# Optimization experiments

Hardware: AMD Instinct MI355X
Metric: run time of the kernel (lower is better)

## Reference

```python
import jax, jax.numpy as jnp
import numpy as np

NL, BS, NQ, D, NH, HD, L, P, DFF, NC = 6, 16, 300, 256, 8, 32, 3, 4, 1024, 80
SHAPES = np.array([[80, 80], [40, 40], [20, 20]], np.int32)  # (H, W) per level: 640x640 input, strides 8/16/32
STARTS = np.array([0, 6400, 8000], np.int32)
LV = 8400  # sum H*W


def setup_inputs():
    keys = iter(jax.random.split(jax.random.key(0), 64))

    def rn(shape, s=0.02):
        return jax.random.normal(next(keys), shape, jnp.float32) * s

    return {
        "tgt": rn((BS, NQ, D), 1.0),
        "ref_points_unact": rn((BS, NQ, 4), 1.0),
        "memory": rn((BS, LV, D), 1.0),
        "spatial_shapes": jnp.asarray(SHAPES),
        "level_start_index": jnp.asarray(STARTS),
        "Wq": rn((NL, D, D)), "bq": rn((NL, D)),
        "Wk": rn((NL, D, D)), "bk": rn((NL, D)),
        "Wv": rn((NL, D, D)), "bv": rn((NL, D)),
        "Wo": rn((NL, D, D)), "bo": rn((NL, D)),
        "ln1_g": jnp.ones((NL, D)), "ln1_b": jnp.zeros((NL, D)),
        "ln2_g": jnp.ones((NL, D)), "ln2_b": jnp.zeros((NL, D)),
        "ln3_g": jnp.ones((NL, D)), "ln3_b": jnp.zeros((NL, D)),
        "Wvp": rn((NL, D, D)), "bvp": rn((NL, D)),
        "Woff": rn((NL, D, NH * L * P * 2)), "boff": rn((NL, NH * L * P * 2), 0.5),
        "Waw": rn((NL, D, NH * L * P)), "baw": rn((NL, NH * L * P)),
        "Wop": rn((NL, D, D)), "bop": rn((NL, D)),
        "Wff1": rn((NL, D, DFF)), "bff1": rn((NL, DFF)),
        "Wff2": rn((NL, DFF, D)), "bff2": rn((NL, D)),
        "Wb1": rn((NL, D, D)), "bb1": rn((NL, D)),
        "Wb2": rn((NL, D, D)), "bb2": rn((NL, D)),
        "Wb3": rn((NL, D, 4)), "bb3": rn((NL, 4)),
        "Ws": rn((NL, D, NC)), "bs_": rn((NL, NC)),
        "Wp1": rn((4, 2 * D)), "bp1": rn((2 * D,)),
        "Wp2": rn((2 * D, D)), "bp2": rn((D,)),
    }


def _ln(x, g, b):
    m = x.mean(-1, keepdims=True)
    v = ((x - m) ** 2).mean(-1, keepdims=True)
    return (x - m) * jax.lax.rsqrt(v + 1e-5) * g + b


def _inv_sigmoid(x, eps=1e-5):
    x = jnp.clip(x, 0.0, 1.0)
    return jnp.log(jnp.clip(x, eps, None)) - jnp.log(jnp.clip(1.0 - x, eps, None))


def _forward(shapes, starts, tgt, ref_points_unact, memory, Wq, bq, Wk, bk, Wv, bv, Wo, bo, ln1_g, ln1_b, ln2_g, ln2_b, ln3_g, ln3_b, Wvp, bvp, Woff, boff, Waw, baw, Wop, bop, Wff1, bff1, Wff2, bff2, Wb1, bb1, Wb2, bb2, Wb3, bb3, Ws, bs_, Wp1, bp1, Wp2, bp2):
    bs, Lq, _ = tgt.shape

    def mha(q, k, v, i):
        qh = (q @ Wq[i] + bq[i]).reshape(bs, Lq, NH, HD)
        kh = (k @ Wk[i] + bk[i]).reshape(bs, Lq, NH, HD)
        vh = (v @ Wv[i] + bv[i]).reshape(bs, Lq, NH, HD)
        att = jax.nn.softmax(jnp.einsum('bqhd,bkhd->bhqk', qh, kh) / np.float32(np.sqrt(HD)), -1)
        return jnp.einsum('bhqk,bkhd->bqhd', att, vh).reshape(bs, Lq, D) @ Wo[i] + bo[i]

    def deform(query, ref, i):
        # multi-scale deformable attention (Deformable-DETR core, bilinear, zero padding)
        val = (memory @ Wvp[i] + bvp[i]).reshape(bs, -1, NH, HD).transpose(0, 2, 1, 3)  # [bs,NH,Lv,HD]
        off = (query @ Woff[i] + boff[i]).reshape(bs, Lq, NH, L, P, 2)
        aw = jax.nn.softmax((query @ Waw[i] + baw[i]).reshape(bs, Lq, NH, L * P), -1).reshape(bs, Lq, NH, L, P)
        r = ref[:, :, None, None, None, :]  # [bs,Lq,1,1,1,4] box (cx,cy,w,h)
        loc = r[..., :2] + off / P * r[..., 2:] * 0.5  # [bs,Lq,NH,L,P,2]
        out = jnp.zeros((bs, NH, Lq, HD), query.dtype)
        for lvl in range(L):
            H, W = int(shapes[lvl, 0]), int(shapes[lvl, 1])
            s = int(starts[lvl])
            vl = val[:, :, s:s + H * W]  # [bs,NH,H*W,HD]
            x = loc[:, :, :, lvl, :, 0].transpose(0, 2, 1, 3) * W - 0.5  # [bs,NH,Lq,P] (align_corners=False)
            y = loc[:, :, :, lvl, :, 1].transpose(0, 2, 1, 3) * H - 0.5
            x0 = jnp.floor(x).astype(jnp.int32)
            y0 = jnp.floor(y).astype(jnp.int32)
            wx, wy = x - x0, y - y0

            def g(xi, yi):
                valid = ((xi >= 0) & (xi < W) & (yi >= 0) & (yi < H)).astype(query.dtype)
                idx = jnp.clip(yi, 0, H - 1) * W + jnp.clip(xi, 0, W - 1)
                gat = jnp.take_along_axis(vl, idx.reshape(bs, NH, Lq * P, 1), axis=2)
                return gat.reshape(bs, NH, Lq, P, HD) * valid[..., None]

            samp = (g(x0, y0) * ((1 - wx) * (1 - wy))[..., None]
                    + g(x0 + 1, y0) * (wx * (1 - wy))[..., None]
                    + g(x0, y0 + 1) * ((1 - wx) * wy)[..., None]
                    + g(x0 + 1, y0 + 1) * (wx * wy)[..., None])
            awl = aw[:, :, :, lvl].transpose(0, 2, 1, 3)  # [bs,NH,Lq,P]
            out = out + (samp * awl[..., None]).sum(3)
        return out.transpose(0, 2, 1, 3).reshape(bs, Lq, D) @ Wop[i] + bop[i]

    ref_d = jax.nn.sigmoid(ref_points_unact)
    out = tgt
    bboxes = logits = None
    for i in range(NL):
        qpos = jax.nn.relu(ref_d @ Wp1 + bp1) @ Wp2 + bp2  # query_pos_head MLP(4 -> 512 -> 256)
        q = out + qpos
        out = _ln(out + mha(q, q, out, i), ln1_g[i], ln1_b[i])
        out = _ln(out + deform(out + qpos, ref_d, i), ln2_g[i], ln2_b[i])
        out = _ln(out + jax.nn.relu(out @ Wff1[i] + bff1[i]) @ Wff2[i] + bff2[i], ln3_g[i], ln3_b[i])
        h = jax.nn.relu(out @ Wb1[i] + bb1[i])
        h = jax.nn.relu(h @ Wb2[i] + bb2[i])
        inter = jax.nn.sigmoid(h @ Wb3[i] + bb3[i] + _inv_sigmoid(ref_d))
        if i == NL - 1:  # eval_idx = -1 -> outputs taken at last layer (inference path)
            bboxes = inter[None]
            logits = (out @ Ws[i] + bs_[i])[None]
        ref_d = inter
    return bboxes, logits


def reference(tgt, ref_points_unact, memory, spatial_shapes, level_start_index, Wq, bq, Wk, bk, Wv, bv, Wo, bo, ln1_g, ln1_b, ln2_g, ln2_b, ln3_g, ln3_b, Wvp, bvp, Woff, boff, Waw, baw, Wop, bop, Wff1, bff1, Wff2, bff2, Wb1, bb1, Wb2, bb2, Wb3, bb3, Ws, bs_, Wp1, bp1, Wp2, bp2):
    shapes = np.asarray(spatial_shapes)
    starts = np.asarray(level_start_index)
    return _forward(shapes, starts, tgt, ref_points_unact, memory, Wq, bq, Wk, bk, Wv, bv, Wo, bo, ln1_g, ln1_b, ln2_g, ln2_b, ln3_g, ln3_b, Wvp, bvp, Woff, boff, Waw, baw, Wop, bop, Wff1, bff1, Wff2, bff2, Wb1, bb1, Wb2, bb2, Wb3, bb3, Ws, bs_, Wp1, bp1, Wp2, bp2)
```

## Files before the change

kernel.cpp:

```cpp
#include <hip/hip_runtime.h>

#define NLAYERS 6
#define BSZ 16
#define NQL 300
#define DM 256
#define NHEAD 8
#define HDIM 32
#define NLVL 3
#define NPT 4
#define DFFN 1024
#define NCLS 80
#define LVTOT 8400
#define NROW (BSZ * NQL)
#define MEMN (BSZ * LVTOT)

typedef __attribute__((ext_vector_type(8))) short bf16x8;
typedef __attribute__((ext_vector_type(8))) ushort us8;
typedef __attribute__((ext_vector_type(4))) float f32x4;

__device__ __forceinline__ float b2f(ushort u) {
    return __uint_as_float(((uint)u) << 16);
}
__device__ __forceinline__ ushort f2b(float f) {
    uint i = __float_as_uint(f);
    uint r = i + 0x7fffu + ((i >> 16) & 1u);
    return (ushort)(r >> 16);
}
__device__ __forceinline__ void split2(float v, ushort& h, ushort& l) {
    ushort hh = f2b(v);
    h = hh;
    l = f2b(v - b2f(hh));
}
__device__ __forceinline__ void gl_lds16(const void* g, void* l) {
    __builtin_amdgcn_global_load_lds(
        (const __attribute__((address_space(1))) unsigned int*)g,
        (__attribute__((address_space(3))) unsigned int*)l, 16, 0, 0);
}

__global__ __launch_bounds__(256) void f2b_kernel(
    const float* __restrict__ src, ushort* __restrict__ dst, int n)
{
    int i = (blockIdx.x * 256 + threadIdx.x) * 4;
    if (i < n) {
        float4 v = *(const float4*)&src[i];
        ushort4 o = {f2b(v.x), f2b(v.y), f2b(v.z), f2b(v.w)};
        *(ushort4*)&dst[i] = o;
    }
}

__global__ __launch_bounds__(256) void split_kernel(
    const float* __restrict__ src, ushort* __restrict__ dh,
    ushort* __restrict__ dl, int n)
{
    int i = (blockIdx.x * 256 + threadIdx.x) * 4;
    if (i < n) {
        float4 v = *(const float4*)&src[i];
        ushort4 h, l;
        split2(v.x, h.x, l.x);
        split2(v.y, h.y, l.y);
        split2(v.z, h.z, l.z);
        split2(v.w, h.w, l.w);
        *(ushort4*)&dh[i] = h;
        *(ushort4*)&dl[i] = l;
    }
}

#define NTE 14
struct TTab {
    const float* s[NTE];
    ushort* d[NTE];
    int K[NTE], N[NTE], dls[NTE], dr0[NTE];
    int tstart[NTE + 1];
};

__global__ __launch_bounds__(256) void transpose_batch_kernel(TTab tab)
{
    __shared__ float tile[32][33];
    const int bx = blockIdx.x;
    int e = 0;
    while (e < NTE - 1 && bx >= tab.tstart[e + 1]) ++e;
    const int local = bx - tab.tstart[e];
    const int K = tab.K[e], N = tab.N[e];
    const int tx_n = (N + 31) >> 5, ty_n = (K + 31) >> 5;
    const int perB = tx_n * ty_n;
    const int z = local / perB;
    const int rem = local - z * perB;
    const int tyi = rem / tx_n, txi = rem - tyi * tx_n;
    const float* src = tab.s[e] + (size_t)z * K * N;
    ushort* dh = tab.d[e] + (size_t)z * tab.dls[e] + (size_t)tab.dr0[e] * K;
    const int n0 = txi * 32, k0 = tyi * 32;
    const int tx = threadIdx.x, ty = threadIdx.y;
    for (int r = 0; r < 32; r += 8) {
        int k = k0 + ty + r, n = n0 + tx;
        if (k < K && n < N) tile[ty + r][tx] = src[(size_t)k * N + n];
    }
    __syncthreads();
    for (int r = 0; r < 32; r += 8) {
        int n = n0 + ty + r, k = k0 + tx;
        if (n < N && k < K) dh[(size_t)n * K + k] = f2b(tile[tx][ty + r]);
    }
}

__global__ __launch_bounds__(256) void concat_both_kernel(
    const float* __restrict__ bq, const float* __restrict__ bk, float* __restrict__ bqk,
    const float* __restrict__ boff, const float* __restrict__ baw, float* __restrict__ bfa)
{
    const int bx = blockIdx.x;
    if (bx < 12) {
        int i = bx * 256 + threadIdx.x;
        if (i < 6 * 512) {
            int l = i / 512, j = i - l * 512;
            bqk[i] = (j < 256) ? bq[l * 256 + j] : bk[l * 256 + j - 256];
        }
    } else {
        int i = (bx - 12) * 256 + threadIdx.x;
        if (i < 6 * 288) {
            int l = i / 288, j = i - l * 288;
            bfa[i] = (j < 192) ? boff[l * 192 + j] : baw[l * 96 + j - 192];
        }
    }
}

template <int ACT>
__global__ __launch_bounds__(256) void gemm_ps(
    const ushort* __restrict__ Ahp, const ushort* __restrict__ Alp,
    const ushort* __restrict__ BTh, const float* __restrict__ bias,
    int M, int N, int K,
    float* __restrict__ Cf, const float* __restrict__ addsrc,
    ushort* __restrict__ Ch, ushort* __restrict__ Cl)
{
    __shared__ __align__(16) ushort Ahs[2][64 * 32];
    __shared__ __align__(16) ushort Als[2][64 * 32];
    __shared__ __align__(16) ushort Bhs[2][64 * 32];

    const int tid  = threadIdx.x;
    const int m0   = blockIdx.x * 64;
    const int n0   = blockIdx.y * 64;
    const int wv   = tid >> 6;
    const int lane = tid & 63;
    const int lm   = lane & 15;
    const int lq   = lane >> 4;
    const int r    = tid >> 2;
    const int c8   = (tid & 3) * 8;

    gl_lds16(&Ahp[(size_t)(m0 + r) * K + c8], &Ahs[0][r * 32 + c8]);
    gl_lds16(&Alp[(size_t)(m0 + r) * K + c8], &Als[0][r * 32 + c8]);
    gl_lds16(&BTh[(size_t)(n0 + r) * K + c8], &Bhs[0][r * 32 + c8]);
    __syncthreads();

    f32x4 acc[4] = {};
    int buf = 0;
    for (int k0 = 32; k0 < K + 32; k0 += 32) {
        const int nxt = buf ^ 1;
        if (k0 < K) {
            gl_lds16(&Ahp[(size_t)(m0 + r) * K + k0 + c8], &Ahs[nxt][r * 32 + c8]);
            gl_lds16(&Alp[(size_t)(m0 + r) * K + k0 + c8], &Als[nxt][r * 32 + c8]);
            gl_lds16(&BTh[(size_t)(n0 + r) * K + k0 + c8], &Bhs[nxt][r * 32 + c8]);
        }
        bf16x8 afh = *(const bf16x8*)&Ahs[buf][(wv * 16 + lm) * 32 + lq * 8];
        bf16x8 afl = *(const bf16x8*)&Als[buf][(wv * 16 + lm) * 32 + lq * 8];
#pragma unroll
        for (int nb = 0; nb < 4; ++nb) {
            bf16x8 bfh = *(const bf16x8*)&Bhs[buf][(nb * 16 + lm) * 32 + lq * 8];
            acc[nb] = __builtin_amdgcn_mfma_f32_16x16x32_bf16(afh, bfh, acc[nb], 0, 0, 0);
            acc[nb] = __builtin_amdgcn_mfma_f32_16x16x32_bf16(afl, bfh, acc[nb], 0, 0, 0);
        }
        __syncthreads();
        buf = nxt;
    }

    const int row = m0 + wv * 16 + lq * 4;
#pragma unroll
    for (int nb = 0; nb < 4; ++nb) {
        int col = n0 + nb * 16 + lm;
        if (col < N) {
            float bv = bias ? bias[col] : 0.f;
#pragma unroll
            for (int rr = 0; rr < 4; ++rr) {
                float v = acc[nb][rr] + bv;
                if (ACT) v = fmaxf(v, 0.f);
                const size_t idx = (size_t)(row + rr) * N + col;
                if (Cf) Cf[idx] = v;
                if (Ch) {
                    float w = addsrc ? (v + addsrc[idx]) : v;
                    ushort h, l;
                    split2(w, h, l);
                    Ch[idx] = h;
                    if (Cl) Cl[idx] = l;
                }
            }
        }
    }
}

__global__ __launch_bounds__(256) void gemm_mix(
    const ushort* __restrict__ Ahp, const ushort* __restrict__ Alp,
    const ushort* __restrict__ BTh, const float* __restrict__ bias,
    int N, int K,
    float* __restrict__ Cf, const float* __restrict__ addsrc,
    ushort* __restrict__ Ch, ushort* __restrict__ Cl,
    int nSmall,
    const ushort* __restrict__ gA, const ushort* __restrict__ gB,
    const float* __restrict__ gbias, ushort* __restrict__ gC,
    int chunkOff)
{
    __shared__ __align__(16) ushort lds[12288];

    const int tid  = threadIdx.x;
    const int wv   = tid >> 6;
    const int lane = tid & 63;
    const int lm   = lane & 15;
    const int lq   = lane >> 4;

    if ((int)blockIdx.x < nSmall) {
        typedef ushort (*lds2)[64 * 32];
        lds2 Ahs = (lds2)lds;
        lds2 Als = (lds2)(lds + 4096);
        lds2 Bhs = (lds2)(lds + 8192);
        const int m0 = (blockIdx.x % 75) * 64;
        const int n0 = (blockIdx.x / 75) * 64;
        const int r  = tid >> 2;
        const int c8 = (tid & 3) * 8;

        gl_lds16(&Ahp[(size_t)(m0 + r) * K + c8], &Ahs[0][r * 32 + c8]);
        gl_lds16(&Alp[(size_t)(m0 + r) * K + c8], &Als[0][r * 32 + c8]);
        gl_lds16(&BTh[(size_t)(n0 + r) * K + c8], &Bhs[0][r * 32 + c8]);
        __syncthreads();

        f32x4 acc[4] = {};
        int buf = 0;
        for (int k0 = 32; k0 < K + 32; k0 += 32) {
            const int nxt = buf ^ 1;
            if (k0 < K) {
                gl_lds16(&Ahp[(size_t)(m0 + r) * K + k0 + c8], &Ahs[nxt][r * 32 + c8]);
                gl_lds16(&Alp[(size_t)(m0 + r) * K + k0 + c8], &Als[nxt][r * 32 + c8]);
                gl_lds16(&BTh[(size_t)(n0 + r) * K + k0 + c8], &Bhs[nxt][r * 32 + c8]);
            }
            bf16x8 afh = *(const bf16x8*)&Ahs[buf][(wv * 16 + lm) * 32 + lq * 8];
            bf16x8 afl = *(const bf16x8*)&Als[buf][(wv * 16 + lm) * 32 + lq * 8];
#pragma unroll
            for (int nb = 0; nb < 4; ++nb) {
                bf16x8 bfh = *(const bf16x8*)&Bhs[buf][(nb * 16 + lm) * 32 + lq * 8];
                acc[nb] = __builtin_amdgcn_mfma_f32_16x16x32_bf16(afh, bfh, acc[nb], 0, 0, 0);
                acc[nb] = __builtin_amdgcn_mfma_f32_16x16x32_bf16(afl, bfh, acc[nb], 0, 0, 0);
            }
            __syncthreads();
            buf = nxt;
        }

        const int row = m0 + wv * 16 + lq * 4;
#pragma unroll
        for (int nb = 0; nb < 4; ++nb) {
            int col = n0 + nb * 16 + lm;
            if (col < N) {
                float bv = bias[col];
#pragma unroll
                for (int rr = 0; rr < 4; ++rr) {
                    float v = acc[nb][rr] + bv;
                    const size_t idx = (size_t)(row + rr) * N + col;
                    if (Cf) Cf[idx] = v;
                    if (Ch) {
                        float w = addsrc ? (v + addsrc[idx]) : v;
                        ushort h, l;
                        split2(w, h, l);
                        Ch[idx] = h;
                        if (Cl) Cl[idx] = l;
                    }
                }
            }
        }
    } else {
        ushort* As = lds;
        ushort* Bs = lds + 4096;
        const int bid = (int)blockIdx.x - nSmall + chunkOff;
        const int n0 = (bid & 1) * 128;
        const int m0 = (bid >> 1) * 128;
        const int wr = wv >> 1, wc = wv & 1;
        const int srow = lane >> 2;
        const int scol = (lane & 3) * 8;

        f32x4 acc[4][4] = {};

        for (int k0 = 0; k0 < 256; k0 += 32) {
            __syncthreads();
#pragma unroll
            for (int s2 = 0; s2 < 2; ++s2) {
                const int seg = wv * 2 + s2;
                const int row = seg * 16 + srow;
                gl_lds16(&gA[(size_t)(m0 + row) * 256 + k0 + scol],
                         &As[seg * 512 + lane * 8]);
                gl_lds16(&gB[(size_t)(n0 + row) * 256 + k0 + scol],
                         &Bs[seg * 512 + lane * 8]);
            }
            __syncthreads();

            bf16x8 af[4], bfr[4];
#pragma unroll
            for (int i = 0; i < 4; ++i)
                af[i] = *(const bf16x8*)&As[(wr * 64 + i * 16 + lm) * 32 + lq * 8];
#pragma unroll
            for (int i = 0; i < 4; ++i)
                bfr[i] = *(const bf16x8*)&Bs[(wc * 64 + i * 16 + lm) * 32 + lq * 8];
#pragma unroll
            for (int mi = 0; mi < 4; ++mi)
#pragma unroll
                for (int ni = 0; ni < 4; ++ni)
                    acc[mi][ni] = __builtin_amdgcn_mfma_f32_16x16x32_bf16(
                        af[mi], bfr[ni], acc[mi][ni], 0, 0, 0);
        }

#pragma unroll
        for (int ni = 0; ni < 4; ++ni) {
            const int col = n0 + wc * 64 + ni * 16 + lm;
            const float bv = gbias[col];
#pragma unroll
            for (int mi = 0; mi < 4; ++mi) {
                const int row = m0 + wr * 64 + mi * 16 + lq * 4;
#pragma unroll
                for (int rr = 0; rr < 4; ++rr)
                    gC[(size_t)(row + rr) * 256 + col] = f2b(acc[mi][ni][rr] + bv);
            }
        }
    }
}

__global__ __launch_bounds__(256) void gemm_qkv(
    const ushort* __restrict__ qhp, const ushort* __restrict__ qlp,
    const ushort* __restrict__ ohp, const ushort* __restrict__ olp,
    const ushort* __restrict__ Bqk, const ushort* __restrict__ Bv,
    const float* __restrict__ biasqk, const float* __restrict__ biasv,
    ushort* __restrict__ Cqk, ushort* __restrict__ Cv)
{
    constexpr int K = 256;
    __shared__ __align__(16) ushort Ahs[2][64 * 32];
    __shared__ __align__(16) ushort Als[2][64 * 32];
    __shared__ __align__(16) ushort Bhs[2][64 * 32];

    const int by = blockIdx.y;
    const ushort *Ahp, *Alp, *BTh;
    const float* bias;
    ushort* Ch;
    int N, n0;
    if (by < 8) { Ahp = qhp; Alp = qlp; BTh = Bqk; bias = biasqk; Ch = Cqk; N = 512; n0 = by * 64; }
    else        { Ahp = ohp; Alp = olp; BTh = Bv;  bias = biasv;  Ch = Cv;  N = 256; n0 = (by - 8) * 64; }

    const int tid  = threadIdx.x;
    const int m0   = blockIdx.x * 64;
    const int wv   = tid >> 6;
    const int lane = tid & 63;
    const int lm   = lane & 15;
    const int lq   = lane >> 4;
    const int r    = tid >> 2;
    const int c8   = (tid & 3) * 8;

    gl_lds16(&Ahp[(size_t)(m0 + r) * K + c8], &Ahs[0][r * 32 + c8]);
    gl_lds16(&Alp[(size_t)(m0 + r) * K + c8], &Als[0][r * 32 + c8]);
    gl_lds16(&BTh[(size_t)(n0 + r) * K + c8], &Bhs[0][r * 32 + c8]);
    __syncthreads();

    f32x4 acc[4] = {};
    int buf = 0;
    for (int k0 = 32; k0 < K + 32; k0 += 32) {
        const int nxt = buf ^ 1;
        if (k0 < K) {
            gl_lds16(&Ahp[(size_t)(m0 + r) * K + k0 + c8], &Ahs[nxt][r * 32 + c8]);
            gl_lds16(&Alp[(size_t)(m0 + r) * K + k0 + c8], &Als[nxt][r * 32 + c8]);
            gl_lds16(&BTh[(size_t)(n0 + r) * K + k0 + c8], &Bhs[nxt][r * 32 + c8]);
        }
        bf16x8 afh = *(const bf16x8*)&Ahs[buf][(wv * 16 + lm) * 32 + lq * 8];
        bf16x8 afl = *(const bf16x8*)&Als[buf][(wv * 16 + lm) * 32 + lq * 8];
#pragma unroll
        for (int nb = 0; nb < 4; ++nb) {
            bf16x8 bfh = *(const bf16x8*)&Bhs[buf][(nb * 16 + lm) * 32 + lq * 8];
            acc[nb] = __builtin_amdgcn_mfma_f32_16x16x32_bf16(afh, bfh, acc[nb], 0, 0, 0);
            acc[nb] = __builtin_amdgcn_mfma_f32_16x16x32_bf16(afl, bfh, acc[nb], 0, 0, 0);
        }
        __syncthreads();
        buf = nxt;
    }

    const int row = m0 + wv * 16 + lq * 4;
#pragma unroll
    for (int nb = 0; nb < 4; ++nb) {
        const int col = n0 + nb * 16 + lm;
        const float bv = bias[col];
#pragma unroll
        for (int rr = 0; rr < 4; ++rr)
            Ch[(size_t)(row + rr) * N + col] = f2b(acc[nb][rr] + bv);
    }
}

__global__ __launch_bounds__(256) void mha_mfma_kernel(
    const ushort* __restrict__ qh, int ldq, const ushort* __restrict__ kh, int ldk,
    const ushort* __restrict__ vh, int ldv,
    ushort* __restrict__ outh, ushort* __restrict__ outl)
{
    __shared__ ushort Kh[304 * 36];
    __shared__ ushort Vth[32 * 328];
    __shared__ ushort Pb[4][16 * 168];

    const int tid = threadIdx.x;
    const int wv = tid >> 6, lane = tid & 63;
    const int bh = blockIdx.x >> 1, half = blockIdx.x & 1;
    const int b = bh >> 3, h = bh & 7;
    const size_t qbase = (size_t)b * NQL * ldq + h * HDIM;
    const size_t kbase = (size_t)b * NQL * ldk + h * HDIM;
    const size_t vbase = (size_t)b * NQL * ldv + h * HDIM;
    const size_t obase = (size_t)b * NQL * DM + h * HDIM;

    for (int idx = tid; idx < 304 * 32; idx += 256) {
        int row = idx >> 5, d = idx & 31;
        Kh[row * 36 + d] = (row < NQL) ? kh[kbase + (size_t)row * ldk + d] : (ushort)0;
    }
    for (int idx = tid; idx < 328 * 32; idx += 256) {
        int key = idx >> 5, d = idx & 31;
        Vth[d * 328 + key] = (key < NQL) ? vh[vbase + (size_t)key * ldv + d] : (ushort)0;
    }
    for (int i = lane; i < 16 * 168; i += 64) Pb[wv][i] = 0;
    __syncthreads();

    const int quad = lane >> 4, c = lane & 15;
    const float scale = 0.17677669529663687f;

    const int qt_beg = (half ? 10 : 0) + wv;
    const int qt_end = (half ? 19 : 10);
    for (int qt = qt_beg; qt < qt_end; qt += 4) {
        const int q = qt * 16 + c;
        bf16x8 qf = *(const bf16x8*)&qh[qbase + (size_t)q * ldq + quad * 8];

        f32x4 sc[19];
#pragma unroll
        for (int kt = 0; kt < 19; ++kt) {
            bf16x8 kf = *(const bf16x8*)&Kh[(kt * 16 + c) * 36 + quad * 8];
            f32x4 a = {};
            a = __builtin_amdgcn_mfma_f32_16x16x32_bf16(qf, kf, a, 0, 0, 0);
            sc[kt] = a;
        }
        float inv4[4];
#pragma unroll
        for (int r = 0; r < 4; ++r) {
            float mx = -1e30f;
#pragma unroll
            for (int kt = 0; kt < 19; ++kt) {
                float s = sc[kt][r] * scale;
                if (kt * 16 + c >= NQL) s = -1e30f;
                sc[kt][r] = s;
                mx = fmaxf(mx, s);
            }
#pragma unroll
            for (int m = 1; m < 16; m <<= 1) mx = fmaxf(mx, __shfl_xor(mx, m, 64));
            float l = 0.f;
#pragma unroll
            for (int kt = 0; kt < 19; ++kt) {
                float p = __expf(sc[kt][r] - mx);
                sc[kt][r] = p;
                l += p;
            }
#pragma unroll
            for (int m = 1; m < 16; m <<= 1) l += __shfl_xor(l, m, 64);
            inv4[r] = 1.f / l;
        }

        f32x4 o0 = {}, o1 = {};
#pragma unroll
        for (int r = 0; r < 4; ++r)
#pragma unroll
            for (int kt = 0; kt < 10; ++kt)
                Pb[wv][(quad * 4 + r) * 168 + kt * 16 + c] = f2b(sc[kt][r] * inv4[r]);
#pragma unroll
        for (int ks = 0; ks < 5; ++ks) {
            bf16x8 pf = *(const bf16x8*)&Pb[wv][c * 168 + ks * 32 + quad * 8];
            bf16x8 v0 = *(const bf16x8*)&Vth[c * 328 + ks * 32 + quad * 8];
            bf16x8 v1 = *(const bf16x8*)&Vth[(16 + c) * 328 + ks * 32 + quad * 8];
            o0 = __builtin_amdgcn_mfma_f32_16x16x32_bf16(pf, v0, o0, 0, 0, 0);
            o1 = __builtin_amdgcn_mfma_f32_16x16x32_bf16(pf, v1, o1, 0, 0, 0);
        }
#pragma unroll
        for (int r = 0; r < 4; ++r) {
#pragma unroll
            for (int kt = 10; kt < 19; ++kt)
                Pb[wv][(quad * 4 + r) * 168 + (kt - 10) * 16 + c] = f2b(sc[kt][r] * inv4[r]);
            Pb[wv][(quad * 4 + r) * 168 + 144 + c] = 0;
        }
#pragma unroll
        for (int ks = 0; ks < 5; ++ks) {
            bf16x8 pf = *(const bf16x8*)&Pb[wv][c * 168 + ks * 32 + quad * 8];
            bf16x8 v0 = *(const bf16x8*)&Vth[c * 328 + 160 + ks * 32 + quad * 8];
            bf16x8 v1 = *(const bf16x8*)&Vth[(16 + c) * 328 + 160 + ks * 32 + quad * 8];
            o0 = __builtin_amdgcn_mfma_f32_16x16x32_bf16(pf, v0, o0, 0, 0, 0);
            o1 = __builtin_amdgcn_mfma_f32_16x16x32_bf16(pf, v1, o1, 0, 0, 0);
        }
#pragma unroll
        for (int r = 0; r < 4; ++r) {
            const int qq = qt * 16 + quad * 4 + r;
            if (qq < NQL) {
                ushort hh, ll;
                split2(o0[r], hh, ll);
                outh[obase + (size_t)qq * DM + c] = hh;
                outl[obase + (size_t)qq * DM + c] = ll;
                split2(o1[r], hh, ll);
                outh[obase + (size_t)qq * DM + 16 + c] = hh;
                outl[obase + (size_t)qq * DM + 16 + c] = ll;
            }
        }
    }
}

__global__ __launch_bounds__(256) void deform_kernel(
    const ushort* __restrict__ val, const float* __restrict__ offaw,
    const float* __restrict__ refd,
    ushort* __restrict__ samph, ushort* __restrict__ sampl)
{
    __shared__ float offs[192];
    __shared__ float aws[96];
    __shared__ float rr[4];
    const int row = blockIdx.x;
    const int b = row / NQL;
    const int t = threadIdx.x;
    if (t < 192) offs[t] = offaw[(size_t)row * 288 + t];
    if (t < 96)  aws[t] = offaw[(size_t)row * 288 + 192 + t];
    if (t < 4)   rr[t] = refd[row * 4 + t];
    __syncthreads();

    const int h = t >> 5, d = t & 31;
    float mx = -1e30f;
#pragma unroll
    for (int j = 0; j < 12; ++j) mx = fmaxf(mx, aws[h * 12 + j]);
    float ev[12]; float se = 0.f;
#pragma unroll
    for (int j = 0; j < 12; ++j) { ev[j] = __expf(aws[h * 12 + j] - mx); se += ev[j]; }
    const float inv = 1.f / se;

    const int HWs[3] = {80, 40, 20};
    const int STs[3] = {0, 6400, 8000};
    float acc = 0.f;
#pragma unroll
    for (int l = 0; l < NLVL; ++l) {
        const int Wd = HWs[l], Hd = HWs[l], st = STs[l];
#pragma unroll
        for (int p = 0; p < NPT; ++p) {
            const float w12 = ev[l * 4 + p] * inv;
            const float ox = offs[((h * 3 + l) * 4 + p) * 2 + 0];
            const float oy = offs[((h * 3 + l) * 4 + p) * 2 + 1];
            const float x = (rr[0] + ox * 0.125f * rr[2]) * Wd - 0.5f;
            const float y = (rr[1] + oy * 0.125f * rr[3]) * Hd - 0.5f;
            const float xf = floorf(x), yf = floorf(y);
            const int x0 = (int)xf, y0 = (int)yf;
            const float wx = x - xf, wy = y - yf;
            const float tw[4] = {(1 - wx) * (1 - wy), wx * (1 - wy),
                                 (1 - wx) * wy,       wx * wy};
            const int xs[4] = {x0, x0 + 1, x0, x0 + 1};
            const int ys[4] = {y0, y0, y0 + 1, y0 + 1};
            float sv = 0.f;
#pragma unroll
            for (int tp = 0; tp < 4; ++tp) {
                const int xi = xs[tp], yi = ys[tp];
                if (xi >= 0 && xi < Wd && yi >= 0 && yi < Hd) {
                    const int idx = st + yi * Wd + xi;
                    sv += tw[tp] * b2f(val[((size_t)b * LVTOT + idx) * DM + h * HDIM + d]);
                }
            }
            acc += w12 * sv;
        }
    }
    ushort hh, ll;
    split2(acc, hh, ll);
    samph[(size_t)row * DM + t] = hh;
    sampl[(size_t)row * DM + t] = ll;
}

__global__ __launch_bounds__(256) void addln_kernel(
    const float* x, const float* __restrict__ dl,
    const float* __restrict__ g, const float* __restrict__ bb,
    float* outf, ushort* __restrict__ outh, ushort* __restrict__ outl,
    const float* __restrict__ qpos, ushort* __restrict__ q2h, ushort* __restrict__ q2l)
{
    const int wv = threadIdx.x >> 6, lane = threadIdx.x & 63;
    const int row = blockIdx.x * 4 + wv;
    const size_t base = (size_t)row * DM + lane * 4;
    const float4 xv = *(const float4*)(x + base);
    const float4 dv = *(const float4*)(dl + base);
    float v[4] = {xv.x + dv.x, xv.y + dv.y, xv.z + dv.z, xv.w + dv.w};

    float s = v[0] + v[1] + v[2] + v[3];
#pragma unroll
    for (int m = 32; m; m >>= 1) s += __shfl_xor(s, m, 64);
    const float mean = s * (1.f / 256.f);
    float sq = 0.f;
#pragma unroll
    for (int j = 0; j < 4; ++j) { float dd = v[j] - mean; sq += dd * dd; }
#pragma unroll
    for (int m = 32; m; m >>= 1) sq += __shfl_xor(sq, m, 64);
    const float rstd = rsqrtf(sq * (1.f / 256.f) + 1e-5f);

    float y[4];
    ushort4 yh, yl;
#pragma unroll
    for (int j = 0; j < 4; ++j) {
        const int col = lane * 4 + j;
        y[j] = (v[j] - mean) * rstd * g[col] + bb[col];
    }
    *(float4*)(outf + base) = make_float4(y[0], y[1], y[2], y[3]);
    split2(y[0], yh.x, yl.x);
    split2(y[1], yh.y, yl.y);
    split2(y[2], yh.z, yl.z);
    split2(y[3], yh.w, yl.w);
    *(ushort4*)(outh + base) = yh;
    *(ushort4*)(outl + base) = yl;
    if (q2h) {
        const float4 qp = *(const float4*)(qpos + base);
        float q2v[4] = {y[0] + qp.x, y[1] + qp.y, y[2] + qp.z, y[3] + qp.w};
        ushort4 qh_, ql_;
        split2(q2v[0], qh_.x, ql_.x);
        split2(q2v[1], qh_.y, ql_.y);
        split2(q2v[2], qh_.z, ql_.z);
        split2(q2v[3], qh_.w, ql_.w);
        *(ushort4*)(q2h + base) = qh_;
        *(ushort4*)(q2l + base) = ql_;
    }
}

__global__ __launch_bounds__(256) void bbox_fused(
    const ushort* __restrict__ h2h, const ushort* __restrict__ h2l,
    const float* __restrict__ Wb3, const float* __restrict__ bb3,
    const float* __restrict__ rpu, float* __restrict__ refd,
    float* __restrict__ dout, int mode, int writeout,
    const float* __restrict__ Wp1, const float* __restrict__ bp1,
    ushort* __restrict__ t1h, ushort* __restrict__ t1l, int computeT1)
{
    __shared__ float hls[64 * 258];
    __shared__ float wb3s[1024];
    __shared__ float wp1s[4 * 512];
    __shared__ float bp1s[512];
    __shared__ float ref4[64 * 4];

    const int tid = threadIdx.x;
    const int r0 = blockIdx.x * 64;

    if (computeT1) {
        for (int i = tid; i < 2048; i += 256) wp1s[i] = Wp1[i];
        if (tid < 256) { bp1s[tid] = bp1[tid]; bp1s[tid + 256] = bp1[tid + 256]; }
    }
    if (mode == 1) {
        for (int i = tid; i < 1024; i += 256) wb3s[i] = Wb3[i];
        for (int j = tid; j < 2048; j += 256) {
            const int row = j >> 5, seg = (j & 31) * 8;
            const size_t g = (size_t)(r0 + row) * 256 + seg;
            us8 hv = *(const us8*)&h2h[g];
            us8 lv = *(const us8*)&h2l[g];
            float* o = &hls[row * 258 + seg];
#pragma unroll
            for (int x = 0; x < 8; ++x) o[x] = b2f(hv[x]) + b2f(lv[x]);
        }
    }
    __syncthreads();

    const int r = tid >> 2, c = tid & 3;
    float v;
    if (mode == 1) {
        float acc = 0.f;
        const float* hrow = &hls[r * 258];
#pragma unroll 4
        for (int k = 0; k < 256; ++k)
            acc = fmaf(hrow[k], wb3s[k * 4 + c], acc);
        const float b3v = acc + bb3[c];
        const float old = refd[(size_t)(r0 + r) * 4 + c];
        const float rc = fminf(fmaxf(old, 0.f), 1.f);
        const float invs = logf(fmaxf(rc, 1e-5f)) - logf(fmaxf(1.f - rc, 1e-5f));
        v = 1.f / (1.f + __expf(-(b3v + invs)));
    } else {
        v = 1.f / (1.f + __expf(-rpu[(size_t)(r0 + r) * 4 + c]));
    }
    refd[(size_t)(r0 + r) * 4 + c] = v;
    if (writeout) dout[(size_t)(r0 + r) * 4 + c] = v;
    ref4[r * 4 + c] = v;
    __syncthreads();

    if (!computeT1) return;
#pragma unroll
    for (int jj = 0; jj < 16; ++jj) {
        const int idx = jj * 2048 + tid * 8;
        const int row = idx >> 9, nb = idx & 511;
        const float a0 = ref4[row * 4 + 0], a1 = ref4[row * 4 + 1];
        const float a2 = ref4[row * 4 + 2], a3 = ref4[row * 4 + 3];
        us8 hv, lv;
#pragma unroll
        for (int x = 0; x < 8; ++x) {
            const int n = nb + x;
            float t = bp1s[n];
            t = fmaf(a0, wp1s[n], t);
            t = fmaf(a1, wp1s[512 + n], t);
            t = fmaf(a2, wp1s[1024 + n], t);
            t = fmaf(a3, wp1s[1536 + n], t);
            t = fmaxf(t, 0.f);
            ushort hh, ll;
            split2(t, hh, ll);
            hv[x] = hh; lv[x] = ll;
        }
        const size_t gg = (size_t)(r0 + row) * 512 + nb;
        *(us8*)&t1h[gg] = hv;
        *(us8*)&t1l[gg] = lv;
    }
}

extern "C" void kernel_launch(void* const* d_in, const int* in_sizes, int n_in,
                              void* d_out, int out_size, void* d_ws, size_t ws_size,
                              hipStream_t stream)
{
    const float* tgt    = (const float*)d_in[0];
    const float* rpu    = (const float*)d_in[1];
    const float* memory = (const float*)d_in[2];
    const float* Wq  = (const float*)d_in[5];  const float* bq  = (const float*)d_in[6];
    const float* Wk  = (const float*)d_in[7];  const float* bk  = (const float*)d_in[8];
    const float* Wv  = (const float*)d_in[9];  const float* bv  = (const float*)d_in[10];
    const float* Wo  = (const float*)d_in[11]; const float* bo  = (const float*)d_in[12];
    const float* ln1g = (const float*)d_in[13]; const float* ln1b = (const float*)d_in[14];
    const float* ln2g = (const float*)d_in[15]; const float* ln2b = (const float*)d_in[16];
    const float* ln3g = (const float*)d_in[17]; const float* ln3b = (const float*)d_in[18];
    const float* Wvp = (const float*)d_in[19]; const float* bvp = (const float*)d_in[20];
    const float* Woff = (const float*)d_in[21]; const float* boff = (const float*)d_in[22];
    const float* Waw = (const float*)d_in[23]; const float* baw = (const float*)d_in[24];
    const float* Wop = (const float*)d_in[25]; const float* bop = (const float*)d_in[26];
    const float* Wff1 = (const float*)d_in[27]; const float* bff1 = (const float*)d_in[28];
    const float* Wff2 = (const float*)d_in[29]; const float* bff2 = (const float*)d_in[30];
    const float* Wb1 = (const float*)d_in[31]; const float* bb1 = (const float*)d_in[32];
    const float* Wb2 = (const float*)d_in[33]; const float* bb2 = (const float*)d_in[34];
    const float* Wb3 = (const float*)d_in[35]; const float* bb3 = (const float*)d_in[36];
    const float* Ws  = (const float*)d_in[37]; const float* bs_ = (const float*)d_in[38];
    const float* Wp1 = (const float*)d_in[39]; const float* bp1 = (const float*)d_in[40];
    const float* Wp2 = (const float*)d_in[41]; const float* bp2 = (const float*)d_in[42];

    size_t off = 0;
    auto alloc = [&](size_t elems, size_t elsz) -> void* {
        void* r = (char*)d_ws + off;
        off += elems * elsz;
        off = (off + 255) & ~(size_t)255;
        return r;
    };
    ushort *wqkh = (ushort*)alloc(6 * 131072, 2);
    ushort *wvh  = (ushort*)alloc(6 * 65536, 2);
    ushort *woh  = (ushort*)alloc(6 * 65536, 2);
    ushort *wvph = (ushort*)alloc(6 * 65536, 2);
    ushort *wfah = (ushort*)alloc(6 * 81920, 2);
    ushort *woph = (ushort*)alloc(6 * 65536, 2);
    ushort *wf1h = (ushort*)alloc(6 * 262144, 2);
    ushort *wf2h = (ushort*)alloc(6 * 262144, 2);
    ushort *wb1h = (ushort*)alloc(6 * 65536, 2);
    ushort *wb2h = (ushort*)alloc(6 * 65536, 2);
    ushort *wsh  = (ushort*)alloc(6 * 20480, 2);
    ushort *wp2h = (ushort*)alloc(131072, 2);
    float  *bqk  = (float*)alloc(6 * 512, 4);
    float  *bfa  = (float*)alloc(6 * 288, 4);

    ushort* mem_bf = (ushort*)alloc((size_t)MEMN * DM, 2);
    ushort* val_bf = (ushort*)alloc((size_t)MEMN * DM, 2);
    float*  out_f  = (float*)alloc(NROW * DM, 4);
    float*  qpos_f = (float*)alloc(NROW * DM, 4);
    float*  tmp_f  = (float*)alloc(NROW * DM, 4);
    float*  refd_f = (float*)alloc(NROW * 4, 4);
    float*  offaw_f = (float*)alloc(NROW * 288, 4);

    ushort* out_h = (ushort*)alloc(NROW * DM, 2);
    ushort* out_l = (ushort*)alloc(NROW * DM, 2);

    const size_t NN = NROW;
    ushort* scratch = (ushort*)alloc(NN * 2056, 2);
    ushort* q_h  = scratch;
    ushort* q_l  = scratch + NN * 256;
    ushort* vh_h = scratch + NN * 512;
    ushort* att_h = scratch;
    ushort* att_l = scratch + NN * 256;
    ushort* q2_h = scratch + NN * 512;
    ushort* q2_l = scratch + NN * 768;
    ushort* samp_h = scratch;
    ushort* samp_l = scratch + NN * 256;
    ushort* ff_h = scratch;
    ushort* ff_l = scratch + NN * 1024;
    ushort* h1_h = scratch;
    ushort* h1_l = scratch + NN * 256;
    ushort* h2_h = scratch + NN * 512;
    ushort* h2_l = scratch + NN * 768;
    ushort* t1_h = scratch + NN * 1024;
    ushort* t1_l = scratch + NN * 1536;
    ushort* qk_h = scratch + NN * 1024;

    if (off > ws_size) return;

    {
        TTab tab;
        const float* ss[NTE] = {Wq, Wk, Wv, Wo, Wvp, Woff, Waw, Wop,
                                Wff1, Wff2, Wb1, Wb2, Ws, Wp2};
        ushort* dd[NTE] = {wqkh, wqkh, wvh, woh, wvph, wfah, wfah, woph,
                           wf1h, wf2h, wb1h, wb2h, wsh, wp2h};
        const int KK[NTE]  = {256, 256, 256, 256, 256, 256, 256, 256,
                              256, 1024, 256, 256, 256, 512};
        const int NNe[NTE] = {256, 256, 256, 256, 256, 192, 96, 256,
                              1024, 256, 256, 256, 80, 256};
        const int BB[NTE]  = {6, 6, 6, 6, 6, 6, 6, 6, 6, 6, 6, 6, 6, 1};
        const int DL[NTE]  = {131072, 131072, 65536, 65536, 65536, 81920, 81920,
                              65536, 262144, 262144, 65536, 65536, 20480, 131072};
        const int DR[NTE]  = {0, 256, 0, 0, 0, 0, 192, 0, 0, 0, 0, 0, 0, 0};
        int total = 0;
        for (int e = 0; e < NTE; ++e) {
            tab.s[e] = ss[e]; tab.d[e] = dd[e];
            tab.K[e] = KK[e]; tab.N[e] = NNe[e];
            tab.dls[e] = DL[e]; tab.dr0[e] = DR[e];
            tab.tstart[e] = total;
            total += ((NNe[e] + 31) / 32) * ((KK[e] + 31) / 32) * BB[e];
        }
        tab.tstart[NTE] = total;
        transpose_batch_kernel<<<total, dim3(32, 8), 0, stream>>>(tab);
    }
    concat_both_kernel<<<19, 256, 0, stream>>>(bq, bk, bqk, boff, baw, bfa);
    f2b_kernel<<<(MEMN * DM) / 1024, 256, 0, stream>>>(memory, mem_bf, MEMN * DM);

    hipMemcpyAsync(out_f, tgt, (size_t)NROW * DM * 4, hipMemcpyDeviceToDevice, stream);
    split_kernel<<<(NROW * DM) / 1024, 256, 0, stream>>>(tgt, out_h, out_l, NROW * DM);
    bbox_fused<<<75, 256, 0, stream>>>(nullptr, nullptr, Wb3, bb3, rpu, refd_f,
                                       nullptr, 0, 0, Wp1, bp1, t1_h, t1_l, 1);

    auto GP = [&](const ushort* Ahp, const ushort* Alp, const ushort* BTh,
                  const float* bias, int N, int K, bool relu,
                  float* Cf, ushort* Ch = nullptr, ushort* Cl = nullptr,
                  const float* addsrc = nullptr) {
        dim3 g(NROW / 64, (N + 63) / 64);
        if (relu) gemm_ps<1><<<g, 256, 0, stream>>>(Ahp, Alp, BTh, bias, NROW, N, K,
                                                    Cf, addsrc, Ch, Cl);
        else      gemm_ps<0><<<g, 256, 0, stream>>>(Ahp, Alp, BTh, bias, NROW, N, K,
                                                    Cf, addsrc, Ch, Cl);
    };

    for (int i = 0; i < NLAYERS; ++i) {
        const ushort* wvp_i = wvph + i * 65536;
        const float*  bvp_i = bvp + i * 256;
        gemm_mix<<<300 + 700, 256, 0, stream>>>(
            t1_h, t1_l, wp2h, bp2, 256, 512, qpos_f, out_f, q_h, q_l,
            300, mem_bf, wvp_i, bvp_i, val_bf, 0);
        gemm_qkv<<<dim3(NROW / 64, 12), 256, 0, stream>>>(
            q_h, q_l, out_h, out_l, wqkh + i * 131072, wvh + i * 65536,
            bqk + i * 512, bv + i * 256, qk_h, vh_h);
        mha_mfma_kernel<<<256, 256, 0, stream>>>(qk_h, 512, qk_h + 256, 512,
                                                 vh_h, 256, att_h, att_l);
        gemm_mix<<<300 + 700, 256, 0, stream>>>(
            att_h, att_l, woh + i * 65536, bo + i * 256, 256, 256, tmp_f,
            nullptr, nullptr, nullptr,
            300, mem_bf, wvp_i, bvp_i, val_bf, 700);
        addln_kernel<<<1200, 256, 0, stream>>>(out_f, tmp_f, ln1g + i * 256, ln1b + i * 256,
                                               out_f, out_h, out_l, qpos_f, q2_h, q2_l);
        gemm_mix<<<375 + 700, 256, 0, stream>>>(
            q2_h, q2_l, wfah + i * 81920, bfa + i * 288, 288, 256, offaw_f,
            nullptr, nullptr, nullptr,
            375, mem_bf, wvp_i, bvp_i, val_bf, 1400);
        deform_kernel<<<4800, 256, 0, stream>>>(val_bf, offaw_f, refd_f, samp_h, samp_l);
        GP(samp_h, samp_l, woph + i * 65536, bop + i * 256, 256, 256, false, tmp_f);
        addln_kernel<<<1200, 256, 0, stream>>>(out_f, tmp_f, ln2g + i * 256, ln2b + i * 256,
                                               out_f, out_h, out_l, nullptr, nullptr, nullptr);
        GP(out_h, out_l, wf1h + i * 262144, bff1 + i * 1024, 1024, 256, true,
           nullptr, ff_h, ff_l);
        GP(ff_h, ff_l, wf2h + i * 262144, bff2 + i * 256, 256, 1024, false, tmp_f);
        addln_kernel<<<1200, 256, 0, stream>>>(out_f, tmp_f, ln3g + i * 256, ln3b + i * 256,
                                               out_f, out_h, out_l, nullptr, nullptr, nullptr);
        GP(out_h, out_l, wb1h + i * 65536, bb1 + i * 256, 256, 256, true,
           nullptr, h1_h, h1_l);
        GP(h1_h, h1_l, wb2h + i * 65536, bb2 + i * 256, 256, 256, true,
           nullptr, h2_h, h2_l);
        const int last = (i == NLAYERS - 1);
        bbox_fused<<<75, 256, 0, stream>>>(h2_h, h2_l, Wb3 + i * 1024, bb3 + i * 4,
                                           nullptr, refd_f, (float*)d_out, 1,
                                           last ? 1 : 0, Wp1, bp1, t1_h, t1_l,
                                           last ? 0 : 1);
        if (last) {
            GP(out_h, out_l, wsh + i * 20480, bs_ + i * 80, 80, 256, false,
               (float*)d_out + NROW * 4);
        }
    }
}
```

Before: 2.097 ms.

## Fuse output GEMMs with residual add and LayerNorm into full-row kernel

```diff
diff --git a/kernel.cpp b/kernel.cpp
--- a/kernel.cpp
+++ b/kernel.cpp
@@ -193,6 +193,120 @@
     }
 }
 
+__global__ __launch_bounds__(256) void gemm_row_ln(
+    const ushort* __restrict__ Ahp, const ushort* __restrict__ Alp,
+    const ushort* __restrict__ BTh, const float* __restrict__ bias,
+    int K,
+    const float* __restrict__ g, const float* __restrict__ bvec,
+    float* outf, ushort* __restrict__ outh, ushort* __restrict__ outl,
+    const float* __restrict__ qpos, ushort* __restrict__ q2h, ushort* __restrict__ q2l)
+{
+    __shared__ __align__(16) ushort Ahs[2][64 * 32];
+    __shared__ __align__(16) ushort Als[2][64 * 32];
+    __shared__ __align__(16) ushort Bhs[2][256 * 32];
+    __shared__ float gls[256], bls[256], bias_ls[256];
+
+    const int tid = threadIdx.x;
+    const int m0 = blockIdx.x * 64;
+    const int wv = tid >> 6, lane = tid & 63;
+    const int lm = lane & 15, lq = lane >> 4;
+    const int r = tid >> 2, c8 = (tid & 3) * 8;
+
+    gls[tid] = g[tid];
+    bls[tid] = bvec[tid];
+    bias_ls[tid] = bias[tid];
+
+    gl_lds16(&Ahp[(size_t)(m0 + r) * K + c8], &Ahs[0][r * 32 + c8]);
+    gl_lds16(&Alp[(size_t)(m0 + r) * K + c8], &Als[0][r * 32 + c8]);
+#pragma unroll
+    for (int j = 0; j < 4; ++j) {
+        const int c = j * 256 + tid;
+        gl_lds16(&BTh[(size_t)(c >> 2) * K + (c & 3) * 8], &Bhs[0][c * 8]);
+    }
+    __syncthreads();
+
+    f32x4 acc[16] = {};
+    int buf = 0;
+    for (int k0 = 32; k0 < K + 32; k0 += 32) {
+        const int nxt = buf ^ 1;
+        if (k0 < K) {
+            gl_lds16(&Ahp[(size_t)(m0 + r) * K + k0 + c8], &Ahs[nxt][r * 32 + c8]);
+            gl_lds16(&Alp[(size_t)(m0 + r) * K + k0 + c8], &Als[nxt][r * 32 + c8]);
+#pragma unroll
+            for (int j = 0; j < 4; ++j) {
+                const int c = j * 256 + tid;
+                gl_lds16(&BTh[(size_t)(c >> 2) * K + k0 + (c & 3) * 8], &Bhs[nxt][c * 8]);
+            }
+        }
+        bf16x8 afh = *(const bf16x8*)&Ahs[buf][(wv * 16 + lm) * 32 + lq * 8];
+        bf16x8 afl = *(const bf16x8*)&Als[buf][(wv * 16 + lm) * 32 + lq * 8];
+#pragma unroll
+        for (int nb = 0; nb < 16; ++nb) {
+            bf16x8 bfh = *(const bf16x8*)&Bhs[buf][(nb * 16 + lm) * 32 + lq * 8];
+            acc[nb] = __builtin_amdgcn_mfma_f32_16x16x32_bf16(afh, bfh, acc[nb], 0, 0, 0);
+            acc[nb] = __builtin_amdgcn_mfma_f32_16x16x32_bf16(afl, bfh, acc[nb], 0, 0, 0);
+        }
+        __syncthreads();
+        buf = nxt;
+    }
+
+    const int rowbase = m0 + wv * 16 + lq * 4;
+    float vsum[4] = {0.f, 0.f, 0.f, 0.f};
+#pragma unroll
+    for (int nb = 0; nb < 16; ++nb) {
+        const int col = nb * 16 + lm;
+        const float bv = bias_ls[col];
+#pragma unroll
+        for (int rr = 0; rr < 4; ++rr) {
+            float v = acc[nb][rr] + bv + outf[(size_t)(rowbase + rr) * DM + col];
+            acc[nb][rr] = v;
+            vsum[rr] += v;
+        }
+    }
+    float mean[4], rstd[4];
+#pragma unroll
+    for (int rr = 0; rr < 4; ++rr) {
+#pragma unroll
+        for (int m = 1; m < 16; m <<= 1) vsum[rr] += __shfl_xor(vsum[rr], m, 64);
+        mean[rr] = vsum[rr] * (1.f / 256.f);
+    }
+    float vsq[4] = {0.f, 0.f, 0.f, 0.f};
+#pragma unroll
+    for (int nb = 0; nb < 16; ++nb)
+#pragma unroll
+        for (int rr = 0; rr < 4; ++rr) {
+            const float d = acc[nb][rr] - mean[rr];
+            vsq[rr] += d * d;
+        }
+#pragma unroll
+    for (int rr = 0; rr < 4; ++rr) {
+#pragma unroll
+        for (int m = 1; m < 16; m <<= 1) vsq[rr] += __shfl_xor(vsq[rr], m, 64);
+        rstd[rr] = rsqrtf(vsq[rr] * (1.f / 256.f) + 1e-5f);
+    }
+#pragma unroll
+    for (int nb = 0; nb < 16; ++nb) {
+        const int col = nb * 16 + lm;
+        const float gv = gls[col], bbv = bls[col];
+#pragma unroll
+        for (int rr = 0; rr < 4; ++rr) {
+            const size_t idx = (size_t)(rowbase + rr) * DM + col;
+            const float y = (acc[nb][rr] - mean[rr]) * rstd[rr] * gv + bbv;
+            outf[idx] = y;
+            ushort hh, ll;
+            split2(y, hh, ll);
+            outh[idx] = hh;
+            outl[idx] = ll;
+            if (q2h) {
+                const float q2v = y + qpos[idx];
+                split2(q2v, hh, ll);
+                q2h[idx] = hh;
+                q2l[idx] = ll;
+            }
+        }
+    }
+}
+
 __global__ __launch_bounds__(256) void gemm_mix(
     const ushort* __restrict__ Ahp, const ushort* __restrict__ Alp,
     const ushort* __restrict__ BTh, const float* __restrict__ bias,
@@ -567,57 +681,6 @@
     split2(acc, hh, ll);
     samph[(size_t)row * DM + t] = hh;
     sampl[(size_t)row * DM + t] = ll;
-}
-
-__global__ __launch_bounds__(256) void addln_kernel(
-    const float* x, const float* __restrict__ dl,
-    const float* __restrict__ g, const float* __restrict__ bb,
-    float* outf, ushort* __restrict__ outh, ushort* __restrict__ outl,
-    const float* __restrict__ qpos, ushort* __restrict__ q2h, ushort* __restrict__ q2l)
-{
-    const int wv = threadIdx.x >> 6, lane = threadIdx.x & 63;
-    const int row = blockIdx.x * 4 + wv;
-    const size_t base = (size_t)row * DM + lane * 4;
-    const float4 xv = *(const float4*)(x + base);
-    const float4 dv = *(const float4*)(dl + base);
-    float v[4] = {xv.x + dv.x, xv.y + dv.y, xv.z + dv.z, xv.w + dv.w};
-
-    float s = v[0] + v[1] + v[2] + v[3];
-#pragma unroll
-    for (int m = 32; m; m >>= 1) s += __shfl_xor(s, m, 64);
-    const float mean = s * (1.f / 256.f);
-    float sq = 0.f;
-#pragma unroll
-    for (int j = 0; j < 4; ++j) { float dd = v[j] - mean; sq += dd * dd; }
-#pragma unroll
-    for (int m = 32; m; m >>= 1) sq += __shfl_xor(sq, m, 64);
-    const float rstd = rsqrtf(sq * (1.f / 256.f) + 1e-5f);
-
-    float y[4];
-    ushort4 yh, yl;
-#pragma unroll
-    for (int j = 0; j < 4; ++j) {
-        const int col = lane * 4 + j;
-        y[j] = (v[j] - mean) * rstd * g[col] + bb[col];
-    }
-    *(float4*)(outf + base) = make_float4(y[0], y[1], y[2], y[3]);
-    split2(y[0], yh.x, yl.x);
-    split2(y[1], yh.y, yl.y);
-    split2(y[2], yh.z, yl.z);
-    split2(y[3], yh.w, yl.w);
-    *(ushort4*)(outh + base) = yh;
-    *(ushort4*)(outl + base) = yl;
-    if (q2h) {
-        const float4 qp = *(const float4*)(qpos + base);
-        float q2v[4] = {y[0] + qp.x, y[1] + qp.y, y[2] + qp.z, y[3] + qp.w};
-        ushort4 qh_, ql_;
-        split2(q2v[0], qh_.x, ql_.x);
-        split2(q2v[1], qh_.y, ql_.y);
-        split2(q2v[2], qh_.z, ql_.z);
-        split2(q2v[3], qh_.w, ql_.w);
-        *(ushort4*)(q2h + base) = qh_;
-        *(ushort4*)(q2l + base) = ql_;
-    }
 }
 
 __global__ __launch_bounds__(256) void bbox_fused(
@@ -756,7 +819,6 @@
     ushort* val_bf = (ushort*)alloc((size_t)MEMN * DM, 2);
     float*  out_f  = (float*)alloc(NROW * DM, 4);
     float*  qpos_f = (float*)alloc(NROW * DM, 4);
-    float*  tmp_f  = (float*)alloc(NROW * DM, 4);
     float*  refd_f = (float*)alloc(NROW * 4, 4);
     float*  offaw_f = (float*)alloc(NROW * 288, 4);
 
@@ -833,7 +895,7 @@
     for (int i = 0; i < NLAYERS; ++i) {
         const ushort* wvp_i = wvph + i * 65536;
         const float*  bvp_i = bvp + i * 256;
-        gemm_mix<<<300 + 700, 256, 0, stream>>>(
+        gemm_mix<<<300 + 1050, 256, 0, stream>>>(
             t1_h, t1_l, wp2h, bp2, 256, 512, qpos_f, out_f, q_h, q_l,
             300, mem_bf, wvp_i, bvp_i, val_bf, 0);
         gemm_qkv<<<dim3(NROW / 64, 12), 256, 0, stream>>>(
@@ -841,25 +903,25 @@
             bqk + i * 512, bv + i * 256, qk_h, vh_h);
         mha_mfma_kernel<<<256, 256, 0, stream>>>(qk_h, 512, qk_h + 256, 512,
                                                  vh_h, 256, att_h, att_l);
-        gemm_mix<<<300 + 700, 256, 0, stream>>>(
-            att_h, att_l, woh + i * 65536, bo + i * 256, 256, 256, tmp_f,
-            nullptr, nullptr, nullptr,
-            300, mem_bf, wvp_i, bvp_i, val_bf, 700);
-        addln_kernel<<<1200, 256, 0, stream>>>(out_f, tmp_f, ln1g + i * 256, ln1b + i * 256,
-                                               out_f, out_h, out_l, qpos_f, q2_h, q2_l);
-        gemm_mix<<<375 + 700, 256, 0, stream>>>(
+        gemm_row_ln<<<75, 256, 0, stream>>>(
+            att_h, att_l, woh + i * 65536, bo + i * 256, 256,
+            ln1g + i * 256, ln1b + i * 256,
+            out_f, out_h, out_l, qpos_f, q2_h, q2_l);
+        gemm_mix<<<375 + 1050, 256, 0, stream>>>(
             q2_h, q2_l, wfah + i * 81920, bfa + i * 288, 288, 256, offaw_f,
             nullptr, nullptr, nullptr,
-            375, mem_bf, wvp_i, bvp_i, val_bf, 1400);
+            375, mem_bf, wvp_i, bvp_i, val_bf, 1050);
         deform_kernel<<<4800, 256, 0, stream>>>(val_bf, offaw_f, refd_f, samp_h, samp_l);
-        GP(samp_h, samp_l, woph + i * 65536, bop + i * 256, 256, 256, false, tmp_f);
-        addln_kernel<<<1200, 256, 0, stream>>>(out_f, tmp_f, ln2g + i * 256, ln2b + i * 256,
-                                               out_f, out_h, out_l, nullptr, nullptr, nullptr);
+        gemm_row_ln<<<75, 256, 0, stream>>>(
+            samp_h, samp_l, woph + i * 65536, bop + i * 256, 256,
+            ln2g + i * 256, ln2b + i * 256,
+            out_f, out_h, out_l, nullptr, nullptr, nullptr);
         GP(out_h, out_l, wf1h + i * 262144, bff1 + i * 1024, 1024, 256, true,
            nullptr, ff_h, ff_l);
-        GP(ff_h, ff_l, wf2h + i * 262144, bff2 + i * 256, 256, 1024, false, tmp_f);
-        addln_kernel<<<1200, 256, 0, stream>>>(out_f, tmp_f, ln3g + i * 256, ln3b + i * 256,
-                                               out_f, out_h, out_l, nullptr, nullptr, nullptr);
+        gemm_row_ln<<<75, 256, 0, stream>>>(
+            ff_h, ff_l, wf2h + i * 262144, bff2 + i * 256, 1024,
+            ln3g + i * 256, ln3b + i * 256,
+            out_f, out_h, out_l, nullptr, nullptr, nullptr);
         GP(out_h, out_l, wb1h + i * 65536, bb1 + i * 256, 256, 256, true,
            nullptr, h1_h, h1_l);
         GP(h1_h, h1_l, wb2h + i * 65536, bb2 + i * 256, 256, 256, true,
```

Measured after the change: 2.303 ms. 9.8% more time.
